# Kernel tuning notes

Hardware: AMD Instinct MI355X
Metric: run time of the kernel (lower is better)

The kernel has to match this reference:

```python
import jax, jax.numpy as jnp
import numpy as np

DIM = 512
HEADS = 8
DIM_HEAD = 64
INNER = HEADS * DIM_HEAD  # 512


def setup_inputs() -> dict:
    key = jax.random.key(0)
    k1, k2, k3 = jax.random.split(key, 3)
    B, N = 4, 2048
    x = jax.random.normal(k1, (B, N, DIM), dtype=jnp.float32)
    # nn.Linear(dim, inner*3, bias=False): weight shape [3*inner, dim]; y = x @ W.T
    w_qkv = jax.random.normal(k2, (3 * INNER, DIM), dtype=jnp.float32) * (DIM ** -0.5)
    # to_out: nn.Linear(inner, dim) with bias
    w_out = jax.random.normal(k3, (DIM, INNER), dtype=jnp.float32) * (INNER ** -0.5)
    b_out = jnp.zeros((DIM,), dtype=jnp.float32)
    return {"x": x, "w_qkv": w_qkv, "w_out": w_out, "b_out": b_out}


def reference(x, w_qkv, w_out, b_out):
    B, N, C = x.shape
    scale = DIM_HEAD ** -0.5
    qkv = jnp.einsum('bnc,fc->bnf', x, w_qkv)  # [B, N, 3*inner]
    qkv = qkv.reshape(B, N, 3, HEADS, DIM_HEAD).transpose(2, 0, 3, 1, 4)  # [3,B,H,N,D]
    q, k, v = qkv[0], qkv[1], qkv[2]
    dots = jnp.einsum('bhnd,bhmd->bhnm', q, k) * scale  # [B,H,N,N]
    attn = jax.nn.softmax(dots, axis=-1)
    out = jnp.einsum('bhnm,bhmd->bhnd', attn, v)  # [B,H,N,D]
    out = out.transpose(0, 2, 1, 3).reshape(B, N, C)
    return jnp.einsum('bnf,cf->bnc', out, w_out) + b_out
```

## Files before the change

### kernel.cpp

```cpp
#include <hip/hip_runtime.h>


typedef __bf16 bf16x8 __attribute__((ext_vector_type(8)));
typedef __bf16 bf16x4v __attribute__((ext_vector_type(4)));
typedef float f32x4 __attribute__((ext_vector_type(4)));
typedef unsigned int u32;
typedef unsigned short u16;
typedef u32 u32x2v __attribute__((ext_vector_type(2)));
typedef u32 u32x4v __attribute__((ext_vector_type(4)));

__device__ __forceinline__ u16 f2bf(float f) {
  union { float f; u32 u; } v; v.f = f;
  u32 r = v.u + 0x7FFFu + ((v.u >> 16) & 1u);
  return (u16)(r >> 16);
}

__device__ __forceinline__ u32x2v pack4bf(float a, float b, float c, float d) {
  bf16x4v v; v[0] = (__bf16)a; v[1] = (__bf16)b; v[2] = (__bf16)c; v[3] = (__bf16)d;
  return __builtin_bit_cast(u32x2v, v);
}

__device__ __forceinline__ f32x4 mfma16(bf16x8 a, bf16x8 b, f32x4 c) {
  return __builtin_amdgcn_mfma_f32_16x16x32_bf16(a, b, c, 0, 0, 0);
}

__global__ void convert_all(const float4* __restrict__ x, const float4* __restrict__ wq,
                            const float4* __restrict__ wo, u16* __restrict__ xb,
                            u16* __restrict__ wqb, u16* __restrict__ wob) {
  int t = blockIdx.x * blockDim.x + threadIdx.x;
  float4 v; u16* dst;
  if (t < 1048576)        { v = x[t];             dst = xb  + (size_t)t * 4; }
  else if (t < 1245184)   { int u = t - 1048576; v = wq[u]; dst = wqb + (size_t)u * 4; }
  else                    { int u = t - 1245184; v = wo[u]; dst = wob + (size_t)u * 4; }
  u32x2v o2;
  o2[0] = (u32)f2bf(v.x) | ((u32)f2bf(v.y) << 16);
  o2[1] = (u32)f2bf(v.z) | ((u32)f2bf(v.w) << 16);
  *(u32x2v*)dst = o2;
}

template<int MODE>
__global__ __launch_bounds__(256, 2) void gemm_nt(
    const u16* __restrict__ A, const u16* __restrict__ B,
    float* __restrict__ Cf, u16* __restrict__ Cb, u16* __restrict__ Vt,
    const float* __restrict__ bias, int M, int N, int K)
{
  __shared__ __align__(16) u16 As[128 * 64];
  __shared__ __align__(16) u16 Bs[128 * 64];
  const int tid = threadIdx.x;
  const int w = tid >> 6, lane = tid & 63, g = lane >> 4, c = lane & 15;
  const int wr = w >> 1, wc = w & 1;
  const int byy = blockIdx.y;
  const int by = (byy & 7) * 8 + (byy >> 3);
  const long m0 = (long)by * 128;
  const long n0 = (long)blockIdx.x * 128;
  const f32x4 zero4 = {0.f, 0.f, 0.f, 0.f};

  f32x4 acc[4][4];
#pragma unroll
  for (int i = 0; i < 4; ++i)
#pragma unroll
    for (int j = 0; j < 4; ++j) acc[i][j] = zero4;

  const int srow = tid >> 3;
  const int sch  = (tid & 7) * 8;

#pragma unroll 1
  for (int kk = 0; kk < K; kk += 64) {
#pragma unroll
    for (int i = 0; i < 4; ++i) {
      __builtin_amdgcn_global_load_lds(
          (__attribute__((address_space(1))) void*)(A + (m0 + i * 32 + srow) * K + kk + sch),
          (__attribute__((address_space(3))) void*)(As + (i * 32 + w * 8) * 64),
          16, 0, 0);
      __builtin_amdgcn_global_load_lds(
          (__attribute__((address_space(1))) void*)(B + (n0 + i * 32 + srow) * K + kk + sch),
          (__attribute__((address_space(3))) void*)(Bs + (i * 32 + w * 8) * 64),
          16, 0, 0);
    }
    __syncthreads();

#pragma unroll
    for (int ks = 0; ks < 2; ++ks) {
      bf16x8 af[4], bfr[4];
#pragma unroll
      for (int mi = 0; mi < 4; ++mi)
        af[mi] = *(const bf16x8*)&As[(wr * 64 + mi * 16 + c) * 64 + ks * 32 + g * 8];
#pragma unroll
      for (int nj = 0; nj < 4; ++nj)
        bfr[nj] = *(const bf16x8*)&Bs[(wc * 64 + nj * 16 + c) * 64 + ks * 32 + g * 8];
#pragma unroll
      for (int mi = 0; mi < 4; ++mi)
#pragma unroll
        for (int nj = 0; nj < 4; ++nj)
          acc[mi][nj] = mfma16(af[mi], bfr[nj], acc[mi][nj]);
    }
    __syncthreads();
  }

#pragma unroll
  for (int mi = 0; mi < 4; ++mi)
#pragma unroll
    for (int nj = 0; nj < 4; ++nj) {
      const long rowb = m0 + wr * 64 + mi * 16 + g * 4;
      const long col  = n0 + wc * 64 + nj * 16 + c;
      if (MODE == 1) {
#pragma unroll
        for (int r = 0; r < 4; ++r)
          Cf[(rowb + r) * N + col] = acc[mi][nj][r] + bias[col];
      } else if (n0 < 512) {
#pragma unroll
        for (int r = 0; r < 4; ++r)
          Cb[(rowb + r) * N + col] = f2bf(acc[mi][nj][r] * 0.18033688f);
      } else if (n0 < 1024) {
#pragma unroll
        for (int r = 0; r < 4; ++r)
          Cb[(rowb + r) * N + col] = f2bf(acc[mi][nj][r]);
      } else {
        u32x2v pk;
        pk[0] = (u32)f2bf(acc[mi][nj][0]) | ((u32)f2bf(acc[mi][nj][1]) << 16);
        pk[1] = (u32)f2bf(acc[mi][nj][2]) | ((u32)f2bf(acc[mi][nj][3]) << 16);
        *(u32x2v*)&Vt[(col - 1024) * 8192 + rowb] = pk;
      }
    }
}

__global__ __launch_bounds__(256, 4) void attn_fwd(const u16* __restrict__ qkv,
                                                   const u16* __restrict__ Vt,
                                                   u16* __restrict__ ao)
{
  __shared__ __align__(16) u16 SH[(32768 + 8192) / 2];
  char* const shb = (char*)SH;

  const int tid = threadIdx.x;
  const int w = tid >> 6, lane = tid & 63, g = lane >> 4, c = lane & 15;

  const int swz = (blockIdx.x & 7) * 128 + (blockIdx.x >> 3);
  const int bh = swz >> 5;
  const int qb = swz & 31;
  const long rowbase = (long)(bh >> 3) * 2048;
  const int hcol = (bh & 7) * 64;
  const int q0 = qb * 64 + w * 16;
  const f32x4 zero4 = {0.f, 0.f, 0.f, 0.f};

  bf16x8 qf[2];
#pragma unroll
  for (int ks = 0; ks < 2; ++ks)
    qf[ks] = *(const bf16x8*)(qkv + (rowbase + q0 + c) * 1536 + hcol + ks * 32 + g * 8);

  float lsum = 0.f;
  f32x4 o[4];
#pragma unroll
  for (int n = 0; n < 4; ++n) o[n] = zero4;

  const u16* kbase = qkv + rowbase * 1536 + 512 + hcol;
  const u16* vtb   = Vt + (long)hcol * 8192 + rowbase;

  const int srow8 = lane >> 3;
  const int schk8 = ((lane & 7) ^ srow8) * 8;
  const int swzc = (c & 7) << 4;

  const int rd0 = c * 128 + ((g * 16) ^ swzc);
  const int rd1 = c * 128 + ((64 + g * 16) ^ swzc);
  const int pr0 = w * 2048 + rd0;
  const int pr1 = w * 2048 + rd1;
  int pwr[4];
#pragma unroll
  for (int n = 0; n < 4; ++n)
    pwr[n] = w * 2048 + c * 128 + ((n * 32 + g * 8) ^ swzc);

  const long r0 = w * 16 + srow8;
  const long r1 = w * 16 + 8 + srow8;
  const u16* kp0 = kbase + (64 + r0) * 1536 + schk8;
  const u16* kp1 = kbase + (64 + r1) * 1536 + schk8;
  const u16* vg0 = vtb + r0 * 8192 + 64 + schk8;
  const u16* vg1 = vtb + r1 * 8192 + 64 + schk8;

  __builtin_amdgcn_global_load_lds(
      (__attribute__((address_space(1))) void*)(kbase + r0 * 1536 + schk8),
      (__attribute__((address_space(3))) void*)(shb + (w * 2 + 0) * 1024), 16, 0, 0);
  __builtin_amdgcn_global_load_lds(
      (__attribute__((address_space(1))) void*)(kbase + r1 * 1536 + schk8),
      (__attribute__((address_space(3))) void*)(shb + (w * 2 + 1) * 1024), 16, 0, 0);
  __builtin_amdgcn_global_load_lds(
      (__attribute__((address_space(1))) void*)(vtb + r0 * 8192 + schk8),
      (__attribute__((address_space(3))) void*)(shb + 16384 + (w * 2 + 0) * 1024), 16, 0, 0);
  __builtin_amdgcn_global_load_lds(
      (__attribute__((address_space(1))) void*)(vtb + r1 * 8192 + schk8),
      (__attribute__((address_space(3))) void*)(shb + 16384 + (w * 2 + 1) * 1024), 16, 0, 0);
  __syncthreads();

  bf16x8 vp[4][2];
  bf16x8 pa[2];

#pragma unroll 2
  for (int t = 0; t < 32; ++t) {
    const int buf = t & 1;
    const int KB = buf * 8192;
    const int VB = 16384 + buf * 8192;
    const int KN = 8192 - KB;
    const int VN = 16384 + (8192 - (VB - 16384));

    if (t < 31) {
      __builtin_amdgcn_global_load_lds(
          (__attribute__((address_space(1))) void*)kp0,
          (__attribute__((address_space(3))) void*)(shb + KN + (w * 2 + 0) * 1024), 16, 0, 0);
      __builtin_amdgcn_global_load_lds(
          (__attribute__((address_space(1))) void*)kp1,
          (__attribute__((address_space(3))) void*)(shb + KN + (w * 2 + 1) * 1024), 16, 0, 0);
      __builtin_amdgcn_global_load_lds(
          (__attribute__((address_space(1))) void*)vg0,
          (__attribute__((address_space(3))) void*)(shb + VN + (w * 2 + 0) * 1024), 16, 0, 0);
      __builtin_amdgcn_global_load_lds(
          (__attribute__((address_space(1))) void*)vg1,
          (__attribute__((address_space(3))) void*)(shb + VN + (w * 2 + 1) * 1024), 16, 0, 0);
      kp0 += 64 * 1536; kp1 += 64 * 1536;
      vg0 += 64;        vg1 += 64;
    }

    if (t > 0) {
      __builtin_amdgcn_s_setprio(1);
#pragma unroll
      for (int ks = 0; ks < 2; ++ks)
#pragma unroll
        for (int n = 0; n < 4; ++n)
          o[n] = mfma16(vp[n][ks], pa[ks], o[n]);
      __builtin_amdgcn_s_setprio(0);
    }

    bf16x8 bk[4][2];
#pragma unroll
    for (int n = 0; n < 4; ++n) {
      bk[n][0] = *(const bf16x8*)(shb + KB + n * 2048 + rd0);
      bk[n][1] = *(const bf16x8*)(shb + KB + n * 2048 + rd1);
    }

    f32x4 s[4];
    __builtin_amdgcn_s_setprio(1);
#pragma unroll
    for (int n = 0; n < 4; ++n) {
      f32x4 a0 = zero4;
      a0 = mfma16(bk[n][0], qf[0], a0);
      a0 = mfma16(bk[n][1], qf[1], a0);
      s[n] = a0;
    }
    __builtin_amdgcn_s_setprio(0);

    float rs = 0.f;
#pragma unroll
    for (int n = 0; n < 4; ++n) {
      float p0 = __builtin_amdgcn_exp2f(s[n][0]);
      float p1 = __builtin_amdgcn_exp2f(s[n][1]);
      float p2 = __builtin_amdgcn_exp2f(s[n][2]);
      float p3 = __builtin_amdgcn_exp2f(s[n][3]);
      rs += (p0 + p1) + (p2 + p3);
      *(u32x2v*)(shb + 32768 + pwr[n]) = pack4bf(p0, p1, p2, p3);
    }
    lsum += rs;

    asm volatile("s_waitcnt lgkmcnt(0)" ::: "memory");
    pa[0] = *(const bf16x8*)(shb + 32768 + pr0);
    pa[1] = *(const bf16x8*)(shb + 32768 + pr1);

#pragma unroll
    for (int n = 0; n < 4; ++n) {
      vp[n][0] = *(const bf16x8*)(shb + VB + n * 2048 + rd0);
      vp[n][1] = *(const bf16x8*)(shb + VB + n * 2048 + rd1);
    }

    __syncthreads();
  }

  __builtin_amdgcn_s_setprio(1);
#pragma unroll
  for (int ks = 0; ks < 2; ++ks)
#pragma unroll
    for (int n = 0; n < 4; ++n)
      o[n] = mfma16(vp[n][ks], pa[ks], o[n]);
  __builtin_amdgcn_s_setprio(0);

  lsum += __shfl_xor(lsum, 16);
  lsum += __shfl_xor(lsum, 32);

  const float linv = 1.0f / lsum;
  u16* aor = ao + (rowbase + q0 + c) * 512 + hcol;
#pragma unroll
  for (int n = 0; n < 4; ++n) {
    u32x2v pk = pack4bf(o[n][0] * linv, o[n][1] * linv, o[n][2] * linv, o[n][3] * linv);
    *(u32x2v*)&aor[n * 16 + g * 4] = pk;
  }
}

extern "C" void kernel_launch(void* const* d_in, const int* in_sizes, int n_in,
                              void* d_out, int out_size, void* d_ws, size_t ws_size,
                              hipStream_t stream) {
  (void)in_sizes; (void)n_in; (void)out_size; (void)ws_size;
  const float* x    = (const float*)d_in[0];
  const float* wqkv = (const float*)d_in[1];
  const float* wout = (const float*)d_in[2];
  const float* bout = (const float*)d_in[3];

  char* ws = (char*)d_ws;
  u16* Xb  = (u16*)(ws);
  u16* Wqb = (u16*)(ws + (8ull << 20));
  u16* Wob = (u16*)(ws + (9ull << 20) + (512ull << 10));
  u16* QKV = (u16*)(ws + (10ull << 20));
  u16* Vt  = (u16*)(ws + (34ull << 20));
  u16* AO  = (u16*)(ws);

  convert_all<<<5120, 256, 0, stream>>>((const float4*)x, (const float4*)wqkv,
                                        (const float4*)wout, Xb, Wqb, Wob);
  gemm_nt<0><<<dim3(12, 64), 256, 0, stream>>>(Xb, Wqb, nullptr, QKV, Vt, nullptr, 8192, 1536, 512);
  attn_fwd<<<1024, 256, 0, stream>>>(QKV, Vt, AO);
  gemm_nt<1><<<dim3(4, 64), 256, 0, stream>>>(AO, Wob, (float*)d_out, nullptr, nullptr, bout, 8192, 512, 512);
}
```

Before: 97.79 us.

## Process two 16-row query subtiles per wave to double K/V reuse

Each wave now computes attention for 32 query rows (two 16-row subtiles) against every loaded K/V tile, doubling the block query tile to 128 and halving the grid. This halves global/LDS traffic for K and V per query and raises the MFMA-to-load ratio. In exchange it increases register usage and P-buffer LDS, lowering occupancy to 2 blocks per CU with fewer waves to hide latency.

```diff
diff --git a/kernel.cpp b/kernel.cpp
--- a/kernel.cpp
+++ b/kernel.cpp
@@ -124,33 +124,37 @@
     }
 }
 
-__global__ __launch_bounds__(256, 4) void attn_fwd(const u16* __restrict__ qkv,
+__global__ __launch_bounds__(256, 2) void attn_fwd(const u16* __restrict__ qkv,
                                                    const u16* __restrict__ Vt,
                                                    u16* __restrict__ ao)
 {
-  __shared__ __align__(16) u16 SH[(32768 + 8192) / 2];
+  __shared__ __align__(16) u16 SH[(32768 + 16384) / 2];
   char* const shb = (char*)SH;
 
   const int tid = threadIdx.x;
   const int w = tid >> 6, lane = tid & 63, g = lane >> 4, c = lane & 15;
 
-  const int swz = (blockIdx.x & 7) * 128 + (blockIdx.x >> 3);
-  const int bh = swz >> 5;
-  const int qb = swz & 31;
+  const int swz = (blockIdx.x & 7) * 64 + (blockIdx.x >> 3);
+  const int bh = swz >> 4;
+  const int qb = swz & 15;
   const long rowbase = (long)(bh >> 3) * 2048;
   const int hcol = (bh & 7) * 64;
-  const int q0 = qb * 64 + w * 16;
+  const int q0 = qb * 128 + w * 32;
   const f32x4 zero4 = {0.f, 0.f, 0.f, 0.f};
 
-  bf16x8 qf[2];
-#pragma unroll
-  for (int ks = 0; ks < 2; ++ks)
-    qf[ks] = *(const bf16x8*)(qkv + (rowbase + q0 + c) * 1536 + hcol + ks * 32 + g * 8);
-
-  float lsum = 0.f;
-  f32x4 o[4];
-#pragma unroll
-  for (int n = 0; n < 4; ++n) o[n] = zero4;
+  bf16x8 qf[2][2];
+#pragma unroll
+  for (int sub = 0; sub < 2; ++sub)
+#pragma unroll
+    for (int ks = 0; ks < 2; ++ks)
+      qf[sub][ks] = *(const bf16x8*)(qkv + (rowbase + q0 + sub * 16 + c) * 1536 + hcol + ks * 32 + g * 8);
+
+  float lsum[2] = {0.f, 0.f};
+  f32x4 o[2][4];
+#pragma unroll
+  for (int sub = 0; sub < 2; ++sub)
+#pragma unroll
+    for (int n = 0; n < 4; ++n) o[sub][n] = zero4;
 
   const u16* kbase = qkv + rowbase * 1536 + 512 + hcol;
   const u16* vtb   = Vt + (long)hcol * 8192 + rowbase;
@@ -161,12 +165,12 @@
 
   const int rd0 = c * 128 + ((g * 16) ^ swzc);
   const int rd1 = c * 128 + ((64 + g * 16) ^ swzc);
-  const int pr0 = w * 2048 + rd0;
-  const int pr1 = w * 2048 + rd1;
+  const int prA0 = w * 4096 + rd0;
+  const int prA1 = w * 4096 + rd1;
   int pwr[4];
 #pragma unroll
   for (int n = 0; n < 4; ++n)
-    pwr[n] = w * 2048 + c * 128 + ((n * 32 + g * 8) ^ swzc);
+    pwr[n] = w * 4096 + c * 128 + ((n * 32 + g * 8) ^ swzc);
 
   const long r0 = w * 16 + srow8;
   const long r1 = w * 16 + 8 + srow8;
@@ -190,7 +194,7 @@
   __syncthreads();
 
   bf16x8 vp[4][2];
-  bf16x8 pa[2];
+  bf16x8 pa[2][2];
 
 #pragma unroll 2
   for (int t = 0; t < 32; ++t) {
@@ -220,10 +224,12 @@
     if (t > 0) {
       __builtin_amdgcn_s_setprio(1);
 #pragma unroll
-      for (int ks = 0; ks < 2; ++ks)
-#pragma unroll
-        for (int n = 0; n < 4; ++n)
-          o[n] = mfma16(vp[n][ks], pa[ks], o[n]);
+      for (int sub = 0; sub < 2; ++sub)
+#pragma unroll
+        for (int ks = 0; ks < 2; ++ks)
+#pragma unroll
+          for (int n = 0; n < 4; ++n)
+            o[sub][n] = mfma16(vp[n][ks], pa[sub][ks], o[sub][n]);
       __builtin_amdgcn_s_setprio(0);
     }
 
@@ -234,32 +240,39 @@
       bk[n][1] = *(const bf16x8*)(shb + KB + n * 2048 + rd1);
     }
 
-    f32x4 s[4];
+    f32x4 s[2][4];
     __builtin_amdgcn_s_setprio(1);
 #pragma unroll
-    for (int n = 0; n < 4; ++n) {
-      f32x4 a0 = zero4;
-      a0 = mfma16(bk[n][0], qf[0], a0);
-      a0 = mfma16(bk[n][1], qf[1], a0);
-      s[n] = a0;
-    }
+    for (int sub = 0; sub < 2; ++sub)
+#pragma unroll
+      for (int n = 0; n < 4; ++n) {
+        f32x4 a0 = zero4;
+        a0 = mfma16(bk[n][0], qf[sub][0], a0);
+        a0 = mfma16(bk[n][1], qf[sub][1], a0);
+        s[sub][n] = a0;
+      }
     __builtin_amdgcn_s_setprio(0);
 
-    float rs = 0.f;
-#pragma unroll
-    for (int n = 0; n < 4; ++n) {
-      float p0 = __builtin_amdgcn_exp2f(s[n][0]);
-      float p1 = __builtin_amdgcn_exp2f(s[n][1]);
-      float p2 = __builtin_amdgcn_exp2f(s[n][2]);
-      float p3 = __builtin_amdgcn_exp2f(s[n][3]);
-      rs += (p0 + p1) + (p2 + p3);
-      *(u32x2v*)(shb + 32768 + pwr[n]) = pack4bf(p0, p1, p2, p3);
-    }
-    lsum += rs;
+#pragma unroll
+    for (int sub = 0; sub < 2; ++sub) {
+      float rs = 0.f;
+#pragma unroll
+      for (int n = 0; n < 4; ++n) {
+        float p0 = __builtin_amdgcn_exp2f(s[sub][n][0]);
+        float p1 = __builtin_amdgcn_exp2f(s[sub][n][1]);
+        float p2 = __builtin_amdgcn_exp2f(s[sub][n][2]);
+        float p3 = __builtin_amdgcn_exp2f(s[sub][n][3]);
+        rs += (p0 + p1) + (p2 + p3);
+        *(u32x2v*)(shb + 32768 + sub * 2048 + pwr[n]) = pack4bf(p0, p1, p2, p3);
+      }
+      lsum[sub] += rs;
+    }
 
     asm volatile("s_waitcnt lgkmcnt(0)" ::: "memory");
-    pa[0] = *(const bf16x8*)(shb + 32768 + pr0);
-    pa[1] = *(const bf16x8*)(shb + 32768 + pr1);
+    pa[0][0] = *(const bf16x8*)(shb + 32768 + prA0);
+    pa[0][1] = *(const bf16x8*)(shb + 32768 + prA1);
+    pa[1][0] = *(const bf16x8*)(shb + 32768 + 2048 + prA0);
+    pa[1][1] = *(const bf16x8*)(shb + 32768 + 2048 + prA1);
 
 #pragma unroll
     for (int n = 0; n < 4; ++n) {
@@ -272,21 +285,27 @@
 
   __builtin_amdgcn_s_setprio(1);
 #pragma unroll
-  for (int ks = 0; ks < 2; ++ks)
-#pragma unroll
-    for (int n = 0; n < 4; ++n)
-      o[n] = mfma16(vp[n][ks], pa[ks], o[n]);
+  for (int sub = 0; sub < 2; ++sub)
+#pragma unroll
+    for (int ks = 0; ks < 2; ++ks)
+#pragma unroll
+      for (int n = 0; n < 4; ++n)
+        o[sub][n] = mfma16(vp[n][ks], pa[sub][ks], o[sub][n]);
   __builtin_amdgcn_s_setprio(0);
 
-  lsum += __shfl_xor(lsum, 16);
-  lsum += __shfl_xor(lsum, 32);
-
-  const float linv = 1.0f / lsum;
-  u16* aor = ao + (rowbase + q0 + c) * 512 + hcol;
-#pragma unroll
-  for (int n = 0; n < 4; ++n) {
-    u32x2v pk = pack4bf(o[n][0] * linv, o[n][1] * linv, o[n][2] * linv, o[n][3] * linv);
-    *(u32x2v*)&aor[n * 16 + g * 4] = pk;
+#pragma unroll
+  for (int sub = 0; sub < 2; ++sub) {
+    float ls = lsum[sub];
+    ls += __shfl_xor(ls, 16);
+    ls += __shfl_xor(ls, 32);
+    const float linv = 1.0f / ls;
+    u16* aor = ao + (rowbase + q0 + sub * 16 + c) * 512 + hcol;
+#pragma unroll
+    for (int n = 0; n < 4; ++n) {
+      u32x2v pk = pack4bf(o[sub][n][0] * linv, o[sub][n][1] * linv,
+                          o[sub][n][2] * linv, o[sub][n][3] * linv);
+      *(u32x2v*)&aor[n * 16 + g * 4] = pk;
+    }
   }
 }
 
@@ -310,6 +329,6 @@
   convert_all<<<5120, 256, 0, stream>>>((const float4*)x, (const float4*)wqkv,
                                         (const float4*)wout, Xb, Wqb, Wob);
   gemm_nt<0><<<dim3(12, 64), 256, 0, stream>>>(Xb, Wqb, nullptr, QKV, Vt, nullptr, 8192, 1536, 512);
-  attn_fwd<<<1024, 256, 0, stream>>>(QKV, Vt, AO);
+  attn_fwd<<<512, 256, 0, stream>>>(QKV, Vt, AO);
   gemm_nt<1><<<dim3(4, 64), 256, 0, stream>>>(AO, Wob, (float*)d_out, nullptr, nullptr, bout, 8192, 512, 512);
 }
```

Result: faster. 93.04 us (-4.9%).
